# Optimization experiments

Measured on AMD Instinct MI355X. Metric: run time of the kernel, lower is better.

## Reference

```python
import jax, jax.numpy as jnp
import numpy as np

B, S, DIM = 2, 2048, 2048
H, DK, DR, DC, DCP, DV = 16, 128, 64, 512, 1024, 128


def setup_inputs() -> dict:
    key = jax.random.key(0)
    ks = jax.random.split(key, 8)
    s = 0.02  # weight init scale
    return {
        "x": jax.random.normal(ks[0], (B, S, DIM), jnp.float32),
        "W_c": jax.random.normal(ks[1], (DIM, DC), jnp.float32) * s,
        "W_c_prime": jax.random.normal(ks[2], (DIM, DCP), jnp.float32) * s,
        "W_qc": jax.random.normal(ks[3], (H, DCP, DK), jnp.float32) * s,
        "W_qr": jax.random.normal(ks[4], (H, DCP, DR), jnp.float32) * s,
        "W_kc": jax.random.normal(ks[5], (H, DC, DK), jnp.float32) * s,
        "W_kr": jax.random.normal(ks[6], (DIM, DR), jnp.float32) * s,
        "W_v": jax.random.normal(ks[7], (H, DC, DV), jnp.float32) * s,
    }


def reference(x, W_c, W_c_prime, W_qc, W_qr, W_kc, W_kr, W_v):
    # Latent compressions
    c = x @ W_c                 # [B,S,DC]  compressed KV latent
    cp = x @ W_c_prime          # [B,S,DCP] compressed Q latent
    # Per-head projections, vectorized over heads
    q_c = jnp.einsum('bsc,hck->bhsk', cp, W_qc)   # [B,H,S,DK]
    q_r = jnp.einsum('bsc,hcr->bhsr', cp, W_qr)   # [B,H,S,DR]
    k_c = jnp.einsum('bsc,hck->bhsk', c, W_kc)    # [B,H,S,DK]
    k_r = x @ W_kr                                 # [B,S,DR] shared across heads
    q = jnp.concatenate([q_c, q_r], axis=-1)                               # [B,H,S,DK+DR]
    k = jnp.concatenate([k_c, jnp.broadcast_to(k_r[:, None], (B, H, S, DR))], axis=-1)
    scale = 1.0 / np.sqrt(DK + DR)
    scores = jnp.einsum('bhsd,bhtd->bhst', q, k) * scale                   # [B,H,S,S]
    causal = jnp.tril(jnp.ones((S, S), dtype=bool))
    scores = jnp.where(causal, scores, -jnp.inf)
    probs = jax.nn.softmax(scores.astype(jnp.float32), axis=-1).astype(q.dtype)
    v = jnp.einsum('bsc,hcv->bhsv', c, W_v)                                # [B,H,S,DV]
    out = jnp.einsum('bhst,bhtv->bhsv', probs, v)                          # [B,H,S,DV]
    return out.transpose(0, 2, 1, 3).reshape(B, S, H * DV)                 # concat heads
```

## Files before the change

### kernel.cpp

```cpp
#include <hip/hip_runtime.h>
#include <stdint.h>

typedef __bf16 bf16;
typedef __bf16 bfx8 __attribute__((ext_vector_type(8)));
typedef __bf16 bfx4 __attribute__((ext_vector_type(4)));
typedef float floatx4 __attribute__((ext_vector_type(4)));

#define B_ 2
#define S_ 2048
#define DIM_ 2048
#define H_ 16
#define DK_ 128
#define DR_ 64
#define DC_ 512
#define DCP_ 1024
#define DV_ 128
#define DQK_ 192

#define MASK_VAL (-30000.0f)
#define C1_ 0.10411754f

__global__ void k_cast(const float* __restrict__ in, bf16* __restrict__ out) {
    size_t i = ((size_t)blockIdx.x * 256 + threadIdx.x) * 8;
    float4 a = *(const float4*)(in + i);
    float4 b = *(const float4*)(in + i + 4);
    bfx8 r;
    r[0] = (bf16)a.x; r[1] = (bf16)a.y; r[2] = (bf16)a.z; r[3] = (bf16)a.w;
    r[4] = (bf16)b.x; r[5] = (bf16)b.y; r[6] = (bf16)b.z; r[7] = (bf16)b.w;
    *(bfx8*)(out + i) = r;
}

__global__ void k_transpose_all(
    const float* __restrict__ W_c, const float* __restrict__ W_cp,
    const float* __restrict__ W_qc, const float* __restrict__ W_qr,
    const float* __restrict__ W_kc, const float* __restrict__ W_kr,
    const float* __restrict__ W_v,
    bf16* __restrict__ Wt_c, bf16* __restrict__ Wt_cp,
    bf16* __restrict__ Wt_qc, bf16* __restrict__ Wt_qr,
    bf16* __restrict__ Wt_kc, bf16* __restrict__ Wt_kr,
    bf16* __restrict__ Wt_v) {
    __shared__ float tile[32][33];
    int bid = blockIdx.x;
    const float* in; bf16* out; int K, N, lx, ly, local;
    if (bid < 1024)      { in = W_c;  out = Wt_c;  K = 2048; N = 512;  lx = 4; ly = 6; local = bid; }
    else if (bid < 3072) { in = W_cp; out = Wt_cp; K = 2048; N = 1024; lx = 5; ly = 6; local = bid - 1024; }
    else if (bid < 5120) { in = W_qc; out = Wt_qc; K = 1024; N = 128;  lx = 2; ly = 5; local = bid - 3072; }
    else if (bid < 6144) { in = W_qr; out = Wt_qr; K = 1024; N = 64;   lx = 1; ly = 5; local = bid - 5120; }
    else if (bid < 7168) { in = W_kc; out = Wt_kc; K = 512;  N = 128;  lx = 2; ly = 4; local = bid - 6144; }
    else if (bid < 7296) { in = W_kr; out = Wt_kr; K = 2048; N = 64;   lx = 1; ly = 6; local = bid - 7168; }
    else                 { in = W_v;  out = Wt_v;  K = 512;  N = 128;  lx = 2; ly = 4; local = bid - 7296; }
    int n0 = (local & ((1 << lx) - 1)) << 5;
    int k0 = ((local >> lx) & ((1 << ly) - 1)) << 5;
    int h  = local >> (lx + ly);
    const float* ip = in + (size_t)h * K * N;
    bf16* op = out + (size_t)h * K * N;
    int tx = threadIdx.x & 31, ty = threadIdx.x >> 5;
#pragma unroll
    for (int i = 0; i < 32; i += 8)
        tile[ty + i][tx] = ip[(size_t)(k0 + ty + i) * N + (n0 + tx)];
    __syncthreads();
#pragma unroll
    for (int i = 0; i < 32; i += 8)
        op[(size_t)(n0 + ty + i) * K + (k0 + tx)] = (bf16)tile[tx][ty + i];
}

__device__ __forceinline__ void gld16(const bf16* g, bf16* l) {
    __builtin_amdgcn_global_load_lds(
        (const __attribute__((address_space(1))) void*)g,
        (__attribute__((address_space(3))) void*)l, 16, 0, 0);
}

__device__ __forceinline__ bfx8 frag_ld(const bf16* lds, int row, int quad) {
    int pb = quad ^ ((row >> 1) & 3);
    return *(const bfx8*)(lds + row * 32 + pb * 8);
}

#define SLICE_ 4096

__device__ __forceinline__ void gemm_core(const bf16* __restrict__ A,
                                          const bf16* __restrict__ Bt,
                                          int K, int rowlimB,
                                          floatx4 acc[4][4],
                                          bf16* A_lds, bf16* B_lds) {
    int tid = threadIdx.x, wave = tid >> 6, lane = tid & 63;
    int l15 = lane & 15, quad = lane >> 4;
    int wm = (wave & 1) * 64, wn = (wave >> 1) * 64;
    int ch0 = wave * 2, ch1 = wave * 2 + 1;
    int r0 = ch0 * 16 + (lane >> 2), r1 = ch1 * 16 + (lane >> 2);
    int kb0 = (lane & 3) ^ ((r0 >> 1) & 3), kb1 = (lane & 3) ^ ((r1 >> 1) & 3);
    int rb0 = r0 <= rowlimB ? r0 : rowlimB;
    int rb1 = r1 <= rowlimB ? r1 : rowlimB;
    const bf16* a0 = A + (size_t)r0 * K + kb0 * 8;
    const bf16* a1 = A + (size_t)r1 * K + kb1 * 8;
    const bf16* b0 = Bt + (size_t)rb0 * K + kb0 * 8;
    const bf16* b1 = Bt + (size_t)rb1 * K + kb1 * 8;
    bf16* da0 = A_lds + ch0 * 512;
    bf16* da1 = A_lds + ch1 * 512;
    bf16* db0 = B_lds + ch0 * 512;
    bf16* db1 = B_lds + ch1 * 512;
    for (int k0 = 0; k0 < K; k0 += 64) {
        __syncthreads();
        gld16(a0 + k0, da0);
        gld16(a1 + k0, da1);
        gld16(b0 + k0, db0);
        gld16(b1 + k0, db1);
        gld16(a0 + k0 + 32, da0 + SLICE_);
        gld16(a1 + k0 + 32, da1 + SLICE_);
        gld16(b0 + k0 + 32, db0 + SLICE_);
        gld16(b1 + k0 + 32, db1 + SLICE_);
        __syncthreads();
#pragma unroll
        for (int sl = 0; sl < 2; ++sl) {
            const bf16* As = A_lds + sl * SLICE_;
            const bf16* Bs = B_lds + sl * SLICE_;
            bfx8 a[4], b[4];
#pragma unroll
            for (int t = 0; t < 4; ++t) a[t] = frag_ld(As, wm + t * 16 + l15, quad);
#pragma unroll
            for (int t = 0; t < 4; ++t) b[t] = frag_ld(Bs, wn + t * 16 + l15, quad);
#pragma unroll
            for (int mt = 0; mt < 4; ++mt)
#pragma unroll
                for (int nt = 0; nt < 4; ++nt)
                    acc[mt][nt] = __builtin_amdgcn_mfma_f32_16x16x32_bf16(
                        a[mt], b[nt], acc[mt][nt], 0, 0, 0);
        }
    }
}

__global__ __launch_bounds__(256, 3) void k_gemm1(
    const bf16* __restrict__ xb, const bf16* __restrict__ Wt_c,
    const bf16* __restrict__ Wt_cp, const bf16* __restrict__ Wt_kr,
    bf16* __restrict__ c_ws, bf16* __restrict__ cp_ws, bf16* __restrict__ kr_ws) {
    __shared__ __attribute__((aligned(16))) bf16 A_lds[2 * SLICE_];
    __shared__ __attribute__((aligned(16))) bf16 B_lds[2 * SLICE_];
    int hw = blockIdx.x + 13 * blockIdx.y;
    int virt = (hw & 7) * 52 + (hw >> 3);
    int bx = virt % 13, by = virt / 13;
    const bf16* Bt; bf16* outp; int ldc, col0, rowlim;
    if (bx < 4)       { Bt = Wt_c  + (size_t)bx * 128 * DIM_;       outp = c_ws;  ldc = DC_;  col0 = bx * 128;       rowlim = 127; }
    else if (bx < 12) { Bt = Wt_cp + (size_t)(bx - 4) * 128 * DIM_; outp = cp_ws; ldc = DCP_; col0 = (bx - 4) * 128; rowlim = 127; }
    else              { Bt = Wt_kr;                                  outp = kr_ws; ldc = DR_;  col0 = 0;              rowlim = 63;  }
    floatx4 acc[4][4];
#pragma unroll
    for (int i = 0; i < 4; ++i)
#pragma unroll
        for (int j = 0; j < 4; ++j) acc[i][j] = (floatx4){0.f, 0.f, 0.f, 0.f};
    gemm_core(xb + (size_t)by * 128 * DIM_, Bt, DIM_, rowlim, acc, A_lds, B_lds);
    int tid = threadIdx.x, wave = tid >> 6, lane = tid & 63;
    int l15 = lane & 15, quad = lane >> 4;
    int wm = (wave & 1) * 64, wn = (wave >> 1) * 64;
#pragma unroll
    for (int mt = 0; mt < 4; ++mt)
#pragma unroll
        for (int nt = 0; nt < 4; ++nt) {
            int n = wn + nt * 16 + l15;
            if (n > rowlim) continue;
#pragma unroll
            for (int r = 0; r < 4; ++r) {
                int m = by * 128 + wm + mt * 16 + quad * 4 + r;
                outp[(size_t)m * ldc + col0 + n] = (bf16)acc[mt][nt][r];
            }
        }
}

__global__ __launch_bounds__(256, 3) void k_gemm2(
    const bf16* __restrict__ cp_ws, const bf16* __restrict__ Wt_qc,
    const bf16* __restrict__ Wt_qr, bf16* __restrict__ q_ws) {
    __shared__ __attribute__((aligned(16))) bf16 A_lds[2 * SLICE_];
    __shared__ __attribute__((aligned(16))) bf16 B_lds[2 * SLICE_];
    int hw = blockIdx.x + 3 * (blockIdx.y + 32 * blockIdx.z);
    int virt = (hw & 7) * 96 + (hw >> 3);
    int bx = virt % 3, by = (virt / 3) & 31, hz = virt / 96;
    const bf16* Bt;
    if (bx < 2) Bt = Wt_qc + (size_t)(hz * 2 + bx) * DK_ * DCP_;
    else        Bt = Wt_qr + (size_t)hz * 128 * DCP_;
    floatx4 acc[4][4];
#pragma unroll
    for (int i = 0; i < 4; ++i)
#pragma unroll
        for (int j = 0; j < 4; ++j) acc[i][j] = (floatx4){0.f, 0.f, 0.f, 0.f};
    gemm_core(cp_ws + (size_t)by * 128 * DCP_, Bt, DCP_, 127, acc, A_lds, B_lds);
    int tid = threadIdx.x, wave = tid >> 6, lane = tid & 63;
    int l15 = lane & 15, quad = lane >> 4;
    int wm = (wave & 1) * 64, wn = (wave >> 1) * 64;
#pragma unroll
    for (int mt = 0; mt < 4; ++mt)
#pragma unroll
        for (int nt = 0; nt < 4; ++nt) {
            int n = wn + nt * 16 + l15;
            int h, col;
            if (bx < 2) { h = hz * 2 + bx;        col = n; }
            else        { h = hz * 2 + (n >> 6);  col = 128 + (n & 63); }
#pragma unroll
            for (int r = 0; r < 4; ++r) {
                int m = by * 128 + wm + mt * 16 + quad * 4 + r;
                int b = m >> 11, s = m & 2047;
                q_ws[(((size_t)b * H_ + h) * S_ + s) * DQK_ + col] =
                    (bf16)(acc[mt][nt][r] * C1_);
            }
        }
}

__global__ __launch_bounds__(256, 3) void k_gemm3(
    const bf16* __restrict__ c_ws, const bf16* __restrict__ Wt_kc,
    const bf16* __restrict__ Wt_v, bf16* __restrict__ kc_ws, bf16* __restrict__ vt_ws) {
    __shared__ __attribute__((aligned(16))) bf16 A_lds[2 * SLICE_];
    __shared__ __attribute__((aligned(16))) bf16 B_lds[2 * SLICE_];
    int hw = blockIdx.x + 2 * (blockIdx.y + 32 * blockIdx.z);
    int virt = (hw & 7) * 128 + (hw >> 3);
    int bx = virt & 1, by = (virt >> 1) & 31, h = virt >> 6;
    const bf16* Bt = (bx == 0) ? (Wt_kc + (size_t)h * DK_ * DC_)
                               : (Wt_v  + (size_t)h * DV_ * DC_);
    floatx4 acc[4][4];
#pragma unroll
    for (int i = 0; i < 4; ++i)
#pragma unroll
        for (int j = 0; j < 4; ++j) acc[i][j] = (floatx4){0.f, 0.f, 0.f, 0.f};
    gemm_core(c_ws + (size_t)by * 128 * DC_, Bt, DC_, 127, acc, A_lds, B_lds);
    int tid = threadIdx.x, wave = tid >> 6, lane = tid & 63;
    int l15 = lane & 15, quad = lane >> 4;
    int wm = (wave & 1) * 64, wn = (wave >> 1) * 64;
#pragma unroll
    for (int mt = 0; mt < 4; ++mt)
#pragma unroll
        for (int nt = 0; nt < 4; ++nt) {
            int n = wn + nt * 16 + l15;
            if (bx == 0) {
#pragma unroll
                for (int r = 0; r < 4; ++r) {
                    int m = by * 128 + wm + mt * 16 + quad * 4 + r;
                    int b = m >> 11, s = m & 2047;
                    kc_ws[(((size_t)b * H_ + h) * S_ + s) * DK_ + n] = (bf16)acc[mt][nt][r];
                }
            } else {
                int m0 = by * 128 + wm + mt * 16 + quad * 4;
                int b = m0 >> 11, s = m0 & 2047;
                bfx4 pack;
#pragma unroll
                for (int r = 0; r < 4; ++r) pack[r] = (bf16)acc[mt][nt][r];
                *(bfx4*)(&vt_ws[(((size_t)b * H_ + h) * DV_ + n) * S_ + s]) = pack;
            }
        }
}

#define KSTR 200
#define VSTR 72
#define PSTR 72

__global__ __launch_bounds__(256, 2) void k_attn(
    const bf16* __restrict__ q_ws, const bf16* __restrict__ kc_ws,
    const bf16* __restrict__ kr_ws, const bf16* __restrict__ vt_ws,
    float* __restrict__ out) {
    __shared__ __attribute__((aligned(16))) bf16 K_lds[64 * KSTR];
    __shared__ __attribute__((aligned(16))) bf16 V_lds[128 * VSTR];
    __shared__ __attribute__((aligned(16))) bf16 P_lds[64 * PSTR];
    int hw = blockIdx.x + 16 * blockIdx.y;
    int virt = (hw & 7) * 64 + (hw >> 3);
    int p = virt & 15;
    int bh = virt >> 4, b = bh >> 4, h = bh & 15;
    int tid = threadIdx.x, wave = tid >> 6, lane = tid & 63;
    int l15 = lane & 15, quad = lane >> 4;

    bf16 ov = (bf16)(l15 == 0 ? 1.f : 0.f);
    bfx8 ones8 = {ov, ov, ov, ov, ov, ov, ov, ov};

    int kn[4], kcc[4], rn[2], rcc[2], vr[4], vcc[4];
#pragma unroll
    for (int i = 0; i < 4; ++i) { int f = (i * 256 + tid) * 8; kn[i] = f >> 7; kcc[i] = f & 127; }
#pragma unroll
    for (int i = 0; i < 2; ++i) { int f = (i * 256 + tid) * 8; rn[i] = f >> 6; rcc[i] = f & 63; }
#pragma unroll
    for (int i = 0; i < 4; ++i) { int f = (i * 256 + tid) * 8; vr[i] = f >> 6; vcc[i] = f & 63; }
    const bf16* kcp[4]; const bf16* krp[2]; const bf16* vp[4];
#pragma unroll
    for (int i = 0; i < 4; ++i) kcp[i] = kc_ws + ((size_t)bh * S_ + kn[i]) * DK_ + kcc[i];
#pragma unroll
    for (int i = 0; i < 2; ++i) krp[i] = kr_ws + ((size_t)b * S_ + rn[i]) * DR_ + rcc[i];
#pragma unroll
    for (int i = 0; i < 4; ++i) vp[i] = vt_ws + ((size_t)bh * DV_ + vr[i]) * S_ + vcc[i];

    for (int ph = 0; ph < 2; ++ph) {
        int qt = ph ? p : 31 - p;
        int q0 = qt * 64, ntiles = qt + 1;

        const bf16* qrow = q_ws + ((size_t)bh * S_ + q0 + wave * 16 + l15) * DQK_;
        bfx8 qf[6];
#pragma unroll
        for (int ks = 0; ks < 6; ++ks)
            qf[ks] = *(const bfx8*)(qrow + ks * 32 + quad * 8);

        floatx4 o_acc[9];
#pragma unroll
        for (int vt = 0; vt < 9; ++vt) o_acc[vt] = (floatx4){0.f, 0.f, 0.f, 0.f};

        bfx8 pk[4], pr[2], pv[4];
#pragma unroll
        for (int i = 0; i < 4; ++i) pk[i] = *(const bfx8*)(kcp[i]);
#pragma unroll
        for (int i = 0; i < 2; ++i) pr[i] = *(const bfx8*)(krp[i]);
#pragma unroll
        for (int i = 0; i < 4; ++i) pv[i] = *(const bfx8*)(vp[i]);

        for (int t = 0; t < ntiles; ++t) {
            __syncthreads();
#pragma unroll
            for (int i = 0; i < 4; ++i) *(bfx8*)(&K_lds[kn[i] * KSTR + kcc[i]]) = pk[i];
#pragma unroll
            for (int i = 0; i < 2; ++i) *(bfx8*)(&K_lds[rn[i] * KSTR + 128 + rcc[i]]) = pr[i];
#pragma unroll
            for (int i = 0; i < 4; ++i) *(bfx8*)(&V_lds[vr[i] * VSTR + vcc[i]]) = pv[i];
            __syncthreads();
            if (t + 1 < ntiles) {
                size_t kv1 = (size_t)(t + 1) * 64;
#pragma unroll
                for (int i = 0; i < 4; ++i) pk[i] = *(const bfx8*)(kcp[i] + kv1 * DK_);
#pragma unroll
                for (int i = 0; i < 2; ++i) pr[i] = *(const bfx8*)(krp[i] + kv1 * DR_);
#pragma unroll
                for (int i = 0; i < 4; ++i) pv[i] = *(const bfx8*)(vp[i] + kv1);
            }
            floatx4 sc[4];
#pragma unroll
            for (int nt = 0; nt < 4; ++nt) sc[nt] = (floatx4){0.f, 0.f, 0.f, 0.f};
            __builtin_amdgcn_s_setprio(1);
#pragma unroll
            for (int ks = 0; ks < 6; ++ks)
#pragma unroll
                for (int nt = 0; nt < 4; ++nt) {
                    bfx8 kf = *(const bfx8*)(&K_lds[(nt * 16 + l15) * KSTR + ks * 32 + quad * 8]);
                    sc[nt] = __builtin_amdgcn_mfma_f32_16x16x32_bf16(qf[ks], kf, sc[nt], 0, 0, 0);
                }
            __builtin_amdgcn_s_setprio(0);
            if (t == ntiles - 1) {
                int kv0 = t * 64;
#pragma unroll
                for (int nt = 0; nt < 4; ++nt)
#pragma unroll
                    for (int r = 0; r < 4; ++r) {
                        int n_g = kv0 + nt * 16 + l15;
                        int q_g = q0 + wave * 16 + quad * 4 + r;
                        if (n_g > q_g) sc[nt][r] = MASK_VAL;
                    }
            }
#pragma unroll
            for (int nt = 0; nt < 4; ++nt)
#pragma unroll
                for (int r = 0; r < 4; ++r)
                    P_lds[(wave * 16 + quad * 4 + r) * PSTR + nt * 16 + l15] =
                        (bf16)exp2f(sc[nt][r]);
            __builtin_amdgcn_s_setprio(1);
#pragma unroll
            for (int ks2 = 0; ks2 < 2; ++ks2) {
                bfx8 pf = *(const bfx8*)(&P_lds[(wave * 16 + l15) * PSTR + ks2 * 32 + quad * 8]);
#pragma unroll
                for (int vt = 0; vt < 8; ++vt) {
                    bfx8 vf = *(const bfx8*)(&V_lds[(vt * 16 + l15) * VSTR + ks2 * 32 + quad * 8]);
                    o_acc[vt] = __builtin_amdgcn_mfma_f32_16x16x32_bf16(pf, vf, o_acc[vt], 0, 0, 0);
                }
                o_acc[8] = __builtin_amdgcn_mfma_f32_16x16x32_bf16(pf, ones8, o_acc[8], 0, 0, 0);
            }
            __builtin_amdgcn_s_setprio(0);
        }
        float rinv[4];
#pragma unroll
        for (int r = 0; r < 4; ++r)
            rinv[r] = 1.f / __shfl(o_acc[8][r], lane & 48);
#pragma unroll
        for (int vt = 0; vt < 8; ++vt)
#pragma unroll
            for (int r = 0; r < 4; ++r) {
                int s = q0 + wave * 16 + quad * 4 + r;
                int v = vt * 16 + l15;
                out[((size_t)b * S_ + s) * (H_ * DV_) + h * DV_ + v] = o_acc[vt][r] * rinv[r];
            }
    }
}

extern "C" void kernel_launch(void* const* d_in, const int* in_sizes, int n_in,
                              void* d_out, int out_size, void* d_ws, size_t ws_size,
                              hipStream_t stream) {
    const float* x    = (const float*)d_in[0];
    const float* W_c  = (const float*)d_in[1];
    const float* W_cp = (const float*)d_in[2];
    const float* W_qc = (const float*)d_in[3];
    const float* W_qr = (const float*)d_in[4];
    const float* W_kc = (const float*)d_in[5];
    const float* W_kr = (const float*)d_in[6];
    const float* W_v  = (const float*)d_in[7];
    float* out = (float*)d_out;

    bf16* c_ws  = (bf16*)d_out;
    bf16* cp_ws = c_ws + (size_t)B_ * S_ * DC_;
    bf16* xb    = cp_ws + (size_t)B_ * S_ * DCP_;

    char* ws = (char*)d_ws;
    size_t off = 0;
    auto alloc = [&](size_t elems) { bf16* p = (bf16*)(ws + off); off += elems * sizeof(bf16); return p; };
    bf16* Wt_c  = alloc((size_t)DIM_ * DC_);
    bf16* Wt_cp = alloc((size_t)DIM_ * DCP_);
    bf16* Wt_qc = alloc((size_t)H_ * DCP_ * DK_);
    bf16* Wt_qr = alloc((size_t)H_ * DCP_ * DR_);
    bf16* Wt_kc = alloc((size_t)H_ * DC_ * DK_);
    bf16* Wt_kr = alloc((size_t)DIM_ * DR_);
    bf16* Wt_v  = alloc((size_t)H_ * DC_ * DV_);
    bf16* kr_ws = alloc((size_t)B_ * S_ * DR_);
    bf16* q_ws  = alloc((size_t)B_ * H_ * S_ * DQK_);
    bf16* kc_ws = alloc((size_t)B_ * H_ * S_ * DK_);
    bf16* vt_ws = alloc((size_t)B_ * H_ * DV_ * S_);

    k_cast<<<dim3(4096), 256, 0, stream>>>(x, xb);
    k_transpose_all<<<dim3(8320), 256, 0, stream>>>(
        W_c, W_cp, W_qc, W_qr, W_kc, W_kr, W_v,
        Wt_c, Wt_cp, Wt_qc, Wt_qr, Wt_kc, Wt_kr, Wt_v);

    k_gemm1<<<dim3(13, 32), 256, 0, stream>>>(xb, Wt_c, Wt_cp, Wt_kr, c_ws, cp_ws, kr_ws);
    k_gemm2<<<dim3(3, 32, 8), 256, 0, stream>>>(cp_ws, Wt_qc, Wt_qr, q_ws);
    k_gemm3<<<dim3(2, 32, H_), 256, 0, stream>>>(c_ws, Wt_kc, Wt_v, kc_ws, vt_ws);
    k_attn<<<dim3(16, B_ * H_), 256, 0, stream>>>(q_ws, kc_ws, kr_ws, vt_ws, out);
}
```

Baseline: 292.5 us.

## Merge prep and mid GEMM launches; swizzle attention LDS layout

Folds the x cast into the weight transpose kernel and merges the Q-projection and K/V-projection GEMMs into one launch, removing two kernel launches and the idle tail between them. The attention kernel's padded K/V/P shared-memory tiles become a dense XOR-swizzled layout read through frag_ld, which cuts LDS footprint and aims to avoid bank conflicts. The merged GEMM mixes two workloads with different K lengths in one grid, which may leave the blocks unevenly balanced.

```diff
diff --git a/kernel.cpp b/kernel.cpp
--- a/kernel.cpp
+++ b/kernel.cpp
@@ -20,17 +20,8 @@
 #define MASK_VAL (-30000.0f)
 #define C1_ 0.10411754f
 
-__global__ void k_cast(const float* __restrict__ in, bf16* __restrict__ out) {
-    size_t i = ((size_t)blockIdx.x * 256 + threadIdx.x) * 8;
-    float4 a = *(const float4*)(in + i);
-    float4 b = *(const float4*)(in + i + 4);
-    bfx8 r;
-    r[0] = (bf16)a.x; r[1] = (bf16)a.y; r[2] = (bf16)a.z; r[3] = (bf16)a.w;
-    r[4] = (bf16)b.x; r[5] = (bf16)b.y; r[6] = (bf16)b.z; r[7] = (bf16)b.w;
-    *(bfx8*)(out + i) = r;
-}
-
-__global__ void k_transpose_all(
+__global__ void k_prep(
+    const float* __restrict__ x, bf16* __restrict__ xb,
     const float* __restrict__ W_c, const float* __restrict__ W_cp,
     const float* __restrict__ W_qc, const float* __restrict__ W_qr,
     const float* __restrict__ W_kc, const float* __restrict__ W_kr,
@@ -40,7 +31,18 @@
     bf16* __restrict__ Wt_kc, bf16* __restrict__ Wt_kr,
     bf16* __restrict__ Wt_v) {
     __shared__ float tile[32][33];
-    int bid = blockIdx.x;
+    int bid0 = blockIdx.x;
+    if (bid0 < 4096) {
+        size_t i = ((size_t)bid0 * 256 + threadIdx.x) * 8;
+        float4 a = *(const float4*)(x + i);
+        float4 b = *(const float4*)(x + i + 4);
+        bfx8 r;
+        r[0] = (bf16)a.x; r[1] = (bf16)a.y; r[2] = (bf16)a.z; r[3] = (bf16)a.w;
+        r[4] = (bf16)b.x; r[5] = (bf16)b.y; r[6] = (bf16)b.z; r[7] = (bf16)b.w;
+        *(bfx8*)(xb + i) = r;
+        return;
+    }
+    int bid = bid0 - 4096;
     const float* in; bf16* out; int K, N, lx, ly, local;
     if (bid < 1024)      { in = W_c;  out = Wt_c;  K = 2048; N = 512;  lx = 4; ly = 6; local = bid; }
     else if (bid < 3072) { in = W_cp; out = Wt_cp; K = 2048; N = 1024; lx = 5; ly = 6; local = bid - 1024; }
@@ -164,97 +166,82 @@
         }
 }
 
-__global__ __launch_bounds__(256, 3) void k_gemm2(
-    const bf16* __restrict__ cp_ws, const bf16* __restrict__ Wt_qc,
-    const bf16* __restrict__ Wt_qr, bf16* __restrict__ q_ws) {
+__global__ __launch_bounds__(256, 3) void k_gemm23(
+    const bf16* __restrict__ cp_ws, const bf16* __restrict__ c_ws,
+    const bf16* __restrict__ Wt_qc, const bf16* __restrict__ Wt_qr,
+    const bf16* __restrict__ Wt_kc, const bf16* __restrict__ Wt_v,
+    bf16* __restrict__ q_ws, bf16* __restrict__ kc_ws, bf16* __restrict__ vt_ws) {
     __shared__ __attribute__((aligned(16))) bf16 A_lds[2 * SLICE_];
     __shared__ __attribute__((aligned(16))) bf16 B_lds[2 * SLICE_];
-    int hw = blockIdx.x + 3 * (blockIdx.y + 32 * blockIdx.z);
-    int virt = (hw & 7) * 96 + (hw >> 3);
-    int bx = virt % 3, by = (virt / 3) & 31, hz = virt / 96;
-    const bf16* Bt;
-    if (bx < 2) Bt = Wt_qc + (size_t)(hz * 2 + bx) * DK_ * DCP_;
-    else        Bt = Wt_qr + (size_t)hz * 128 * DCP_;
-    floatx4 acc[4][4];
-#pragma unroll
-    for (int i = 0; i < 4; ++i)
-#pragma unroll
-        for (int j = 0; j < 4; ++j) acc[i][j] = (floatx4){0.f, 0.f, 0.f, 0.f};
-    gemm_core(cp_ws + (size_t)by * 128 * DCP_, Bt, DCP_, 127, acc, A_lds, B_lds);
+    int hw = blockIdx.x;
+    int virt = (hw & 7) * 224 + (hw >> 3);
     int tid = threadIdx.x, wave = tid >> 6, lane = tid & 63;
     int l15 = lane & 15, quad = lane >> 4;
     int wm = (wave & 1) * 64, wn = (wave >> 1) * 64;
-#pragma unroll
-    for (int mt = 0; mt < 4; ++mt)
-#pragma unroll
-        for (int nt = 0; nt < 4; ++nt) {
-            int n = wn + nt * 16 + l15;
-            int h, col;
-            if (bx < 2) { h = hz * 2 + bx;        col = n; }
-            else        { h = hz * 2 + (n >> 6);  col = 128 + (n & 63); }
-#pragma unroll
-            for (int r = 0; r < 4; ++r) {
-                int m = by * 128 + wm + mt * 16 + quad * 4 + r;
-                int b = m >> 11, s = m & 2047;
-                q_ws[(((size_t)b * H_ + h) * S_ + s) * DQK_ + col] =
-                    (bf16)(acc[mt][nt][r] * C1_);
-            }
-        }
-}
-
-__global__ __launch_bounds__(256, 3) void k_gemm3(
-    const bf16* __restrict__ c_ws, const bf16* __restrict__ Wt_kc,
-    const bf16* __restrict__ Wt_v, bf16* __restrict__ kc_ws, bf16* __restrict__ vt_ws) {
-    __shared__ __attribute__((aligned(16))) bf16 A_lds[2 * SLICE_];
-    __shared__ __attribute__((aligned(16))) bf16 B_lds[2 * SLICE_];
-    int hw = blockIdx.x + 2 * (blockIdx.y + 32 * blockIdx.z);
-    int virt = (hw & 7) * 128 + (hw >> 3);
-    int bx = virt & 1, by = (virt >> 1) & 31, h = virt >> 6;
-    const bf16* Bt = (bx == 0) ? (Wt_kc + (size_t)h * DK_ * DC_)
-                               : (Wt_v  + (size_t)h * DV_ * DC_);
     floatx4 acc[4][4];
 #pragma unroll
     for (int i = 0; i < 4; ++i)
 #pragma unroll
         for (int j = 0; j < 4; ++j) acc[i][j] = (floatx4){0.f, 0.f, 0.f, 0.f};
-    gemm_core(c_ws + (size_t)by * 128 * DC_, Bt, DC_, 127, acc, A_lds, B_lds);
-    int tid = threadIdx.x, wave = tid >> 6, lane = tid & 63;
-    int l15 = lane & 15, quad = lane >> 4;
-    int wm = (wave & 1) * 64, wn = (wave >> 1) * 64;
-#pragma unroll
-    for (int mt = 0; mt < 4; ++mt)
-#pragma unroll
-        for (int nt = 0; nt < 4; ++nt) {
-            int n = wn + nt * 16 + l15;
-            if (bx == 0) {
+    if (virt < 768) {
+        int bx = virt % 3, by = (virt / 3) & 31, hz = virt / 96;
+        const bf16* Bt;
+        if (bx < 2) Bt = Wt_qc + (size_t)(hz * 2 + bx) * DK_ * DCP_;
+        else        Bt = Wt_qr + (size_t)hz * 128 * DCP_;
+        gemm_core(cp_ws + (size_t)by * 128 * DCP_, Bt, DCP_, 127, acc, A_lds, B_lds);
+#pragma unroll
+        for (int mt = 0; mt < 4; ++mt)
+#pragma unroll
+            for (int nt = 0; nt < 4; ++nt) {
+                int n = wn + nt * 16 + l15;
+                int h, col;
+                if (bx < 2) { h = hz * 2 + bx;        col = n; }
+                else        { h = hz * 2 + (n >> 6);  col = 128 + (n & 63); }
 #pragma unroll
                 for (int r = 0; r < 4; ++r) {
                     int m = by * 128 + wm + mt * 16 + quad * 4 + r;
                     int b = m >> 11, s = m & 2047;
-                    kc_ws[(((size_t)b * H_ + h) * S_ + s) * DK_ + n] = (bf16)acc[mt][nt][r];
+                    q_ws[(((size_t)b * H_ + h) * S_ + s) * DQK_ + col] =
+                        (bf16)(acc[mt][nt][r] * C1_);
                 }
-            } else {
-                int m0 = by * 128 + wm + mt * 16 + quad * 4;
-                int b = m0 >> 11, s = m0 & 2047;
-                bfx4 pack;
-#pragma unroll
-                for (int r = 0; r < 4; ++r) pack[r] = (bf16)acc[mt][nt][r];
-                *(bfx4*)(&vt_ws[(((size_t)b * H_ + h) * DV_ + n) * S_ + s]) = pack;
-            }
-        }
-}
-
-#define KSTR 200
-#define VSTR 72
-#define PSTR 72
+            }
+    } else {
+        int v2 = virt - 768;
+        int bx = v2 & 1, by = (v2 >> 1) & 31, h = v2 >> 6;
+        const bf16* Bt = (bx == 0) ? (Wt_kc + (size_t)h * DK_ * DC_)
+                                   : (Wt_v  + (size_t)h * DV_ * DC_);
+        gemm_core(c_ws + (size_t)by * 128 * DC_, Bt, DC_, 127, acc, A_lds, B_lds);
+#pragma unroll
+        for (int mt = 0; mt < 4; ++mt)
+#pragma unroll
+            for (int nt = 0; nt < 4; ++nt) {
+                int n = wn + nt * 16 + l15;
+                if (bx == 0) {
+#pragma unroll
+                    for (int r = 0; r < 4; ++r) {
+                        int m = by * 128 + wm + mt * 16 + quad * 4 + r;
+                        int b = m >> 11, s = m & 2047;
+                        kc_ws[(((size_t)b * H_ + h) * S_ + s) * DK_ + n] = (bf16)acc[mt][nt][r];
+                    }
+                } else {
+                    int m0 = by * 128 + wm + mt * 16 + quad * 4;
+                    int b = m0 >> 11, s = m0 & 2047;
+                    bfx4 pack;
+#pragma unroll
+                    for (int r = 0; r < 4; ++r) pack[r] = (bf16)acc[mt][nt][r];
+                    *(bfx4*)(&vt_ws[(((size_t)b * H_ + h) * DV_ + n) * S_ + s]) = pack;
+                }
+            }
+    }
+}
 
 __global__ __launch_bounds__(256, 2) void k_attn(
     const bf16* __restrict__ q_ws, const bf16* __restrict__ kc_ws,
     const bf16* __restrict__ kr_ws, const bf16* __restrict__ vt_ws,
     float* __restrict__ out) {
-    __shared__ __attribute__((aligned(16))) bf16 K_lds[64 * KSTR];
-    __shared__ __attribute__((aligned(16))) bf16 V_lds[128 * VSTR];
-    __shared__ __attribute__((aligned(16))) bf16 P_lds[64 * PSTR];
+    __shared__ __attribute__((aligned(16))) bf16 K_lds[6 * 2048];
+    __shared__ __attribute__((aligned(16))) bf16 V_lds[2 * 4096];
+    __shared__ __attribute__((aligned(16))) bf16 P_lds[2 * 2048];
     int hw = blockIdx.x + 16 * blockIdx.y;
     int virt = (hw & 7) * 64 + (hw >> 3);
     int p = virt & 15;
@@ -265,20 +252,20 @@
     bf16 ov = (bf16)(l15 == 0 ? 1.f : 0.f);
     bfx8 ones8 = {ov, ov, ov, ov, ov, ov, ov, ov};
 
-    int kn[4], kcc[4], rn[2], rcc[2], vr[4], vcc[4];
-#pragma unroll
-    for (int i = 0; i < 4; ++i) { int f = (i * 256 + tid) * 8; kn[i] = f >> 7; kcc[i] = f & 127; }
-#pragma unroll
-    for (int i = 0; i < 2; ++i) { int f = (i * 256 + tid) * 8; rn[i] = f >> 6; rcc[i] = f & 63; }
-#pragma unroll
-    for (int i = 0; i < 4; ++i) { int f = (i * 256 + tid) * 8; vr[i] = f >> 6; vcc[i] = f & 63; }
+    int rowk = tid >> 2;
+    int kb   = (tid & 3) ^ ((tid >> 3) & 3);
     const bf16* kcp[4]; const bf16* krp[2]; const bf16* vp[4];
 #pragma unroll
-    for (int i = 0; i < 4; ++i) kcp[i] = kc_ws + ((size_t)bh * S_ + kn[i]) * DK_ + kcc[i];
-#pragma unroll
-    for (int i = 0; i < 2; ++i) krp[i] = kr_ws + ((size_t)b * S_ + rn[i]) * DR_ + rcc[i];
-#pragma unroll
-    for (int i = 0; i < 4; ++i) vp[i] = vt_ws + ((size_t)bh * DV_ + vr[i]) * S_ + vcc[i];
+    for (int j = 0; j < 4; ++j)
+        kcp[j] = kc_ws + ((size_t)bh * S_ + rowk) * DK_ + j * 32 + kb * 8;
+#pragma unroll
+    for (int j = 0; j < 2; ++j)
+        krp[j] = kr_ws + ((size_t)b * S_ + rowk) * DR_ + j * 32 + kb * 8;
+#pragma unroll
+    for (int j = 0; j < 4; ++j)
+        vp[j] = vt_ws + ((size_t)bh * DV_ + (j & 1) * 64 + rowk) * S_ + (j >> 1) * 32 + kb * 8;
+    bf16* kdst = K_lds + (size_t)tid * 8;
+    bf16* vdst = V_lds + (size_t)tid * 8;
 
     for (int ph = 0; ph < 2; ++ph) {
         int qt = ph ? p : 31 - p;
@@ -296,29 +283,29 @@
 
         bfx8 pk[4], pr[2], pv[4];
 #pragma unroll
-        for (int i = 0; i < 4; ++i) pk[i] = *(const bfx8*)(kcp[i]);
-#pragma unroll
-        for (int i = 0; i < 2; ++i) pr[i] = *(const bfx8*)(krp[i]);
-#pragma unroll
-        for (int i = 0; i < 4; ++i) pv[i] = *(const bfx8*)(vp[i]);
+        for (int j = 0; j < 4; ++j) pk[j] = *(const bfx8*)(kcp[j]);
+#pragma unroll
+        for (int j = 0; j < 2; ++j) pr[j] = *(const bfx8*)(krp[j]);
+#pragma unroll
+        for (int j = 0; j < 4; ++j) pv[j] = *(const bfx8*)(vp[j]);
 
         for (int t = 0; t < ntiles; ++t) {
             __syncthreads();
 #pragma unroll
-            for (int i = 0; i < 4; ++i) *(bfx8*)(&K_lds[kn[i] * KSTR + kcc[i]]) = pk[i];
-#pragma unroll
-            for (int i = 0; i < 2; ++i) *(bfx8*)(&K_lds[rn[i] * KSTR + 128 + rcc[i]]) = pr[i];
-#pragma unroll
-            for (int i = 0; i < 4; ++i) *(bfx8*)(&V_lds[vr[i] * VSTR + vcc[i]]) = pv[i];
+            for (int j = 0; j < 4; ++j) *(bfx8*)(kdst + j * 2048) = pk[j];
+#pragma unroll
+            for (int j = 0; j < 2; ++j) *(bfx8*)(kdst + (4 + j) * 2048) = pr[j];
+#pragma unroll
+            for (int j = 0; j < 4; ++j) *(bfx8*)(vdst + j * 2048) = pv[j];
             __syncthreads();
             if (t + 1 < ntiles) {
                 size_t kv1 = (size_t)(t + 1) * 64;
 #pragma unroll
-                for (int i = 0; i < 4; ++i) pk[i] = *(const bfx8*)(kcp[i] + kv1 * DK_);
-#pragma unroll
-                for (int i = 0; i < 2; ++i) pr[i] = *(const bfx8*)(krp[i] + kv1 * DR_);
-#pragma unroll
-                for (int i = 0; i < 4; ++i) pv[i] = *(const bfx8*)(vp[i] + kv1);
+                for (int j = 0; j < 4; ++j) pk[j] = *(const bfx8*)(kcp[j] + kv1 * DK_);
+#pragma unroll
+                for (int j = 0; j < 2; ++j) pr[j] = *(const bfx8*)(krp[j] + kv1 * DR_);
+#pragma unroll
+                for (int j = 0; j < 4; ++j) pv[j] = *(const bfx8*)(vp[j] + kv1);
             }
             floatx4 sc[4];
 #pragma unroll
@@ -328,7 +315,7 @@
             for (int ks = 0; ks < 6; ++ks)
 #pragma unroll
                 for (int nt = 0; nt < 4; ++nt) {
-                    bfx8 kf = *(const bfx8*)(&K_lds[(nt * 16 + l15) * KSTR + ks * 32 + quad * 8]);
+                    bfx8 kf = frag_ld(K_lds + ks * 2048, nt * 16 + l15, quad);
                     sc[nt] = __builtin_amdgcn_mfma_f32_16x16x32_bf16(qf[ks], kf, sc[nt], 0, 0, 0);
                 }
             __builtin_amdgcn_s_setprio(0);
@@ -346,16 +333,20 @@
 #pragma unroll
             for (int nt = 0; nt < 4; ++nt)
 #pragma unroll
-                for (int r = 0; r < 4; ++r)
-                    P_lds[(wave * 16 + quad * 4 + r) * PSTR + nt * 16 + l15] =
+                for (int r = 0; r < 4; ++r) {
+                    int prow = wave * 16 + quad * 4 + r;
+                    int pcol = nt * 16 + l15;
+                    P_lds[(nt >> 1) * 2048 + prow * 32 +
+                          ((((pcol >> 3) & 3) ^ ((prow >> 1) & 3)) * 8) + (pcol & 7)] =
                         (bf16)exp2f(sc[nt][r]);
+                }
             __builtin_amdgcn_s_setprio(1);
 #pragma unroll
             for (int ks2 = 0; ks2 < 2; ++ks2) {
-                bfx8 pf = *(const bfx8*)(&P_lds[(wave * 16 + l15) * PSTR + ks2 * 32 + quad * 8]);
+                bfx8 pf = frag_ld(P_lds + ks2 * 2048, wave * 16 + l15, quad);
 #pragma unroll
                 for (int vt = 0; vt < 8; ++vt) {
-                    bfx8 vf = *(const bfx8*)(&V_lds[(vt * 16 + l15) * VSTR + ks2 * 32 + quad * 8]);
+                    bfx8 vf = frag_ld(V_lds + ks2 * 4096, vt * 16 + l15, quad);
                     o_acc[vt] = __builtin_amdgcn_mfma_f32_16x16x32_bf16(pf, vf, o_acc[vt], 0, 0, 0);
                 }
                 o_acc[8] = __builtin_amdgcn_mfma_f32_16x16x32_bf16(pf, ones8, o_acc[8], 0, 0, 0);
@@ -409,13 +400,12 @@
     bf16* kc_ws = alloc((size_t)B_ * H_ * S_ * DK_);
     bf16* vt_ws = alloc((size_t)B_ * H_ * DV_ * S_);
 
-    k_cast<<<dim3(4096), 256, 0, stream>>>(x, xb);
-    k_transpose_all<<<dim3(8320), 256, 0, stream>>>(
-        W_c, W_cp, W_qc, W_qr, W_kc, W_kr, W_v,
+    k_prep<<<dim3(12416), 256, 0, stream>>>(
+        x, xb, W_c, W_cp, W_qc, W_qr, W_kc, W_kr, W_v,
         Wt_c, Wt_cp, Wt_qc, Wt_qr, Wt_kc, Wt_kr, Wt_v);
 
     k_gemm1<<<dim3(13, 32), 256, 0, stream>>>(xb, Wt_c, Wt_cp, Wt_kr, c_ws, cp_ws, kr_ws);
-    k_gemm2<<<dim3(3, 32, 8), 256, 0, stream>>>(cp_ws, Wt_qc, Wt_qr, q_ws);
-    k_gemm3<<<dim3(2, 32, H_), 256, 0, stream>>>(c_ws, Wt_kc, Wt_v, kc_ws, vt_ws);
+    k_gemm23<<<dim3(1792), 256, 0, stream>>>(cp_ws, c_ws, Wt_qc, Wt_qr, Wt_kc, Wt_v,
+                                             q_ws, kc_ws, vt_ws);
     k_attn<<<dim3(16, B_ * H_), 256, 0, stream>>>(q_ws, kc_ws, kr_ws, vt_ws, out);
 }
```

New measurement: 294.4 us. About the same (+0.7%).
